# Optimization experiments

Hardware: AMD Instinct MI355X
Metric: run time of the kernel (lower is better)

The kernel has to match this reference:

```python
import jax, jax.numpy as jnp
import numpy as np

L, B, S, D, H, E = 3, 2, 2048, 1024, 16, 4
Dh = D // H  # 64
DF = E * D   # 4096


def _ln(x, g, b, eps=1e-5):
    m = jnp.mean(x, axis=-1, keepdims=True)
    v = jnp.mean(jnp.square(x - m), axis=-1, keepdims=True)
    return (x - m) * jax.lax.rsqrt(v + eps) * g + b


def setup_inputs() -> dict:
    key = jax.random.key(0)
    ks = jax.random.split(key, 12)
    s = 0.02
    f32 = jnp.float32
    return {
        "x":    jax.random.normal(ks[0], (B, S, D), f32),
        "Wq":   jax.random.normal(ks[1], (L, Dh, Dh), f32) * s,
        "Wk":   jax.random.normal(ks[2], (L, Dh, Dh), f32) * s,
        "Wv":   jax.random.normal(ks[3], (L, Dh, Dh), f32) * s,
        "Wo":   jax.random.normal(ks[4], (L, D, D), f32) * s,
        "bo":   jnp.zeros((L, D), f32),
        "ln1_g": jnp.ones((L, D), f32),
        "ln1_b": jnp.zeros((L, D), f32),
        "W1":   jax.random.normal(ks[5], (L, DF, D), f32) * s,
        "b1":   jnp.zeros((L, DF), f32),
        "W2":   jax.random.normal(ks[6], (L, D, DF), f32) * s,
        "b2":   jnp.zeros((L, D), f32),
        "ln2_g": jnp.ones((L, D), f32),
        "ln2_b": jnp.zeros((L, D), f32),
    }


def reference(x, Wq, Wk, Wv, Wo, bo, ln1_g, ln1_b, W1, b1, W2, b2, ln2_g, ln2_b):
    scale = 1.0 / np.sqrt(Dh).astype(np.float32)
    out = x
    for l in range(L):
        xh = out.reshape(B, S, H, Dh)
        # per-head Linear (shared 64x64 weight across heads), torch Linear: y = x @ W.T
        q = jnp.einsum('bshd,ed->bhse', xh, Wq[l])  # [B,H,S,Dh]
        k = jnp.einsum('bshd,ed->bhse', xh, Wk[l])
        v = jnp.einsum('bshd,ed->bhse', xh, Wv[l])
        att = jax.nn.softmax(jnp.einsum('bhse,bhte->bhst', q, k) * scale, axis=-1)
        ctx = jnp.einsum('bhst,bhtd->bshd', att, v).reshape(B, S, D)
        att_out = ctx @ Wo[l].T + bo[l]
        n1 = _ln(att_out + out, ln1_g[l], ln1_b[l])  # residual adds layer input (v == out)
        ff = jax.nn.relu(n1 @ W1[l].T + b1[l]) @ W2[l].T + b2[l]
        out = _ln(ff + n1, ln2_g[l], ln2_b[l])
    return out
```

## Files before the change

### kernel.cpp

```cpp
#include <hip/hip_runtime.h>
#include <hip/hip_bf16.h>
#include <math.h>


#define DEVINL __device__ __forceinline__
typedef unsigned short ushort_t;
using short8 = __attribute__((ext_vector_type(8))) short;
using f32x4  = __attribute__((ext_vector_type(4))) float;

#if defined(__has_builtin)
#if __has_builtin(__builtin_amdgcn_exp2f)
#define EXPFN(x) __builtin_amdgcn_exp2f(x)
#define QSCALE 0.18033688011112042f
#define HAVE_EXP2 1
#endif
#endif
#ifndef HAVE_EXP2
#define EXPFN(x) __expf(x)
#define QSCALE 0.125f
#endif

DEVINL short f2b(float f) {
  unsigned u = __float_as_uint(f);
  u += 0x7fff + ((u >> 16) & 1);
  return (short)(u >> 16);
}
DEVINL unsigned pk2(float a, float b) {
  unsigned ua = __float_as_uint(a), ub = __float_as_uint(b);
  ua += 0x7fff + ((ua >> 16) & 1);
  ub += 0x7fff + ((ub >> 16) & 1);
  return (ua >> 16) | (ub & 0xffff0000u);
}
DEVINL unsigned pkc(float a, float b) {
  float2 f; f.x = a; f.y = b;
  __hip_bfloat162 h = __float22bfloat162_rn(f);
  return *reinterpret_cast<unsigned*>(&h);
}
DEVINL float bl(unsigned u) { return __uint_as_float(u << 16); }
DEVINL float bh(unsigned u) { return __uint_as_float(u & 0xffff0000u); }
DEVINL f32x4 mfma16(short8 a, short8 b, f32x4 c) {
  return __builtin_amdgcn_mfma_f32_16x16x32_bf16(a, b, c, 0, 0, 0);
}

typedef __attribute__((address_space(3))) void lds_void;
typedef __attribute__((address_space(1))) void gbl_void;
DEVINL void gl16(const void* g, void* l) {
  __builtin_amdgcn_global_load_lds((const gbl_void*)(unsigned long long)g,
                                   (lds_void*)(unsigned long long)l, 16, 0, 0);
}
template <int N> DEVINL void waitvm() {
  asm volatile("s_waitcnt vmcnt(%0)" ::"n"(N) : "memory");
}
DEVINL void barrier_raw() { __builtin_amdgcn_s_barrier(); }
DEVINL void sched0() { __builtin_amdgcn_sched_barrier(0); }

__global__ __launch_bounds__(256)
void conv_bf16(const float* __restrict__ src, ushort_t* __restrict__ dst,
               int n8) {
  int i = blockIdx.x * 256 + threadIdx.x;
  const int stride = gridDim.x * 256;
  for (; i < n8; i += stride) {
    float4 a = ((const float4*)src)[2 * i];
    float4 b = ((const float4*)src)[2 * i + 1];
    uint4 o;
    o.x = pk2(a.x, a.y); o.y = pk2(a.z, a.w);
    o.z = pk2(b.x, b.y); o.w = pk2(b.z, b.w);
    ((uint4*)dst)[i] = o;
  }
}

DEVINL float block_sum(float v, float* red) {
#pragma unroll
  for (int off = 32; off > 0; off >>= 1) v += __shfl_xor(v, off, 64);
  if ((threadIdx.x & 63) == 0) red[threadIdx.x >> 6] = v;
  __syncthreads();
  float r = red[0] + red[1] + red[2] + red[3];
  __syncthreads();
  return r;
}

__global__ __launch_bounds__(256)
void ln_dual2(const ushort_t* __restrict__ pa, const ushort_t* __restrict__ pb,
              const float* __restrict__ bias, const float* __restrict__ R,
              const float* __restrict__ g, const float* __restrict__ b,
              float* __restrict__ outf, ushort_t* __restrict__ outb) {
  __shared__ float red[4];
  const size_t base = (size_t)blockIdx.x * 1024 + threadIdx.x * 4;
  uint2 ua = *(const uint2*)(pa + base);
  uint2 ub = *(const uint2*)(pb + base);
  float4 vr = *(const float4*)(R + base);
  float4 vbi = *(const float4*)(bias + threadIdx.x * 4);
  float4 v;
  v.x = bl(ua.x) + bl(ub.x) + vr.x + vbi.x;
  v.y = bh(ua.x) + bh(ub.x) + vr.y + vbi.y;
  v.z = bl(ua.y) + bl(ub.y) + vr.z + vbi.z;
  v.w = bh(ua.y) + bh(ub.y) + vr.w + vbi.w;
  float s = block_sum(v.x + v.y + v.z + v.w, red);
  float mean = s * (1.0f / 1024.0f);
  float dx = v.x - mean, dy = v.y - mean, dz = v.z - mean, dw = v.w - mean;
  float sq = block_sum(dx * dx + dy * dy + dz * dz + dw * dw, red);
  float rstd = rsqrtf(sq * (1.0f / 1024.0f) + 1e-5f);
  const float4 gv = *(const float4*)(g + threadIdx.x * 4);
  const float4 bv = *(const float4*)(b + threadIdx.x * 4);
  float4 o;
  o.x = dx * rstd * gv.x + bv.x;
  o.y = dy * rstd * gv.y + bv.y;
  o.z = dz * rstd * gv.z + bv.z;
  o.w = dw * rstd * gv.w + bv.w;
  *(float4*)(outf + base) = o;
  uint2 p;
  p.x = pk2(o.x, o.y); p.y = pk2(o.z, o.w);
  *(uint2*)(outb + base) = p;
}

template <int BM, int BN, int WR, int WC, bool OBF, int EPI, bool SWZ>
__global__ __launch_bounds__(WR * WC * 64)
void gemm_db(const ushort_t* __restrict__ A, const ushort_t* __restrict__ W,
             const float* __restrict__ bias, void* __restrict__ Cp, int M,
             int N, int Klen, int lda, int ldw) {
  constexpr int THREADS = WR * WC * 64;
  constexpr int FM = BM / WR / 16;
  constexpr int FN = BN / WC / 16;
  constexpr int CA = BM * 8 / THREADS;
  constexpr int CB = BN * 8 / THREADS;
  constexpr int L = CA + CB;
  __shared__ __align__(16) ushort_t As[2][BM * 64];
  __shared__ __align__(16) ushort_t Bs[2][BN * 64];
  const int tid = threadIdx.x;
  const int lane = tid & 63, lo = lane & 15, hi = lane >> 4, w = tid >> 6;
  int bx = blockIdx.x, by = blockIdx.y;
  if (SWZ) {
    int id = by * gridDim.x + bx;
    const int cpx = (gridDim.x * gridDim.y) >> 3;
    id = (id & 7) * cpx + (id >> 3);
    bx = id % gridDim.x;
    by = id / gridDim.x;
  }
  const int m0 = by * BM, n0 = bx * BN;
  const int wm = (w / WC) * (BM / WR), wn = (w % WC) * (BN / WC);
  const int kbase = blockIdx.z * Klen;

  auto stage = [&](int t, int buf) {
    const int k0 = kbase + t * 64;
#pragma unroll
    for (int i = 0; i < CA; ++i) {
      const int c = i * THREADS + tid;
      const int r = c >> 3, sg = (c & 7) ^ (r & 7);
      gl16(A + (size_t)(m0 + r) * lda + k0 + sg * 8, &As[buf][c * 8]);
    }
#pragma unroll
    for (int i = 0; i < CB; ++i) {
      const int c = i * THREADS + tid;
      const int r = c >> 3, sg = (c & 7) ^ (r & 7);
      gl16(W + (size_t)(n0 + r) * ldw + k0 + sg * 8, &Bs[buf][c * 8]);
    }
  };

  f32x4 acc[FM][FN] = {};
  auto compute = [&](int cur) {
#pragma unroll
    for (int ks = 0; ks < 2; ++ks) {
      short8 af[FM], bf_[FN];
#pragma unroll
      for (int fm = 0; fm < FM; ++fm) {
        const int row = wm + fm * 16 + lo;
        af[fm] = *(const short8*)
            &As[cur][row * 64 + (((ks * 4 + hi) ^ (row & 7)) << 3)];
      }
#pragma unroll
      for (int fn = 0; fn < FN; ++fn) {
        const int row = wn + fn * 16 + lo;
        bf_[fn] = *(const short8*)
            &Bs[cur][row * 64 + (((ks * 4 + hi) ^ (row & 7)) << 3)];
      }
#pragma unroll
      for (int fm = 0; fm < FM; ++fm)
#pragma unroll
        for (int fn = 0; fn < FN; ++fn)
          acc[fm][fn] = mfma16(af[fm], bf_[fn], acc[fm][fn]);
    }
  };

  const int nt = Klen / 64;
  stage(0, 0);
  for (int t = 0; t < nt - 1; ++t) {
    const int cur = t & 1;
    stage(t + 1, cur ^ 1);
    waitvm<L>();
    barrier_raw(); sched0();
    compute(cur);
    barrier_raw(); sched0();
  }
  waitvm<0>();
  barrier_raw(); sched0();
  compute((nt - 1) & 1);

  float bv[FN];
#pragma unroll
  for (int fn = 0; fn < FN; ++fn)
    bv[fn] = (EPI & 1) ? bias[n0 + wn + fn * 16 + lo] : 0.f;
#pragma unroll
  for (int fm = 0; fm < FM; ++fm)
#pragma unroll
    for (int fn = 0; fn < FN; ++fn) {
      const int col = n0 + wn + fn * 16 + lo;
#pragma unroll
      for (int r = 0; r < 4; ++r) {
        const int row = m0 + wm + fm * 16 + hi * 4 + r;
        float v = acc[fm][fn][r] + bv[fn];
        if (EPI & 4) v = fmaxf(v, 0.f);
        if (OBF) {
          ushort_t* Cb = (ushort_t*)Cp + (size_t)blockIdx.z * M * N;
          Cb[(size_t)row * N + col] = (ushort_t)f2b(v);
        } else {
          float* Cf = (float*)Cp + (size_t)blockIdx.z * M * N;
          Cf[(size_t)row * N + col] = v;
        }
      }
    }
}

__global__ __launch_bounds__(256)
void qkv_kernel(const ushort_t* __restrict__ A, const ushort_t* __restrict__ Wq,
                const ushort_t* __restrict__ Wk, const ushort_t* __restrict__ Wv,
                ushort_t* __restrict__ q, ushort_t* __restrict__ k,
                ushort_t* __restrict__ v) {
  __shared__ __align__(16) ushort_t As[128 * 64];
  __shared__ __align__(16) ushort_t Ws[3][64 * 64];
  const int tid = threadIdx.x;
  const int lane = tid & 63, lo = lane & 15, hi = lane >> 4, w = tid >> 6;
  const int m0 = blockIdx.x * 128;
  const int wm = (w >> 1) * 64, wn = (w & 1) * 32;

#pragma unroll
  for (int i = 0; i < 4; ++i) {
    const int c = i * 256 + tid;
    const int r = c >> 3, sg = (c & 7) ^ (r & 7);
    gl16(A + (size_t)(m0 + r) * 64 + sg * 8, As + c * 8);
  }
#pragma unroll
  for (int o = 0; o < 3; ++o) {
    const ushort_t* wb = (o == 0) ? Wq : (o == 1) ? Wk : Wv;
#pragma unroll
    for (int i = 0; i < 2; ++i) {
      const int c = i * 256 + tid;
      const int r = c >> 3, sg = (c & 7) ^ (r & 7);
      gl16(wb + (size_t)r * 64 + sg * 8, Ws[o] + c * 8);
    }
  }
  __syncthreads();

#pragma unroll
  for (int o = 0; o < 3; ++o) {
    ushort_t* ob = (o == 0) ? q : (o == 1) ? k : v;
    const float sc = (o == 0) ? QSCALE : 1.0f;
    f32x4 acc[4][2] = {};
#pragma unroll
    for (int ks = 0; ks < 2; ++ks) {
      short8 af[4], bf[2];
#pragma unroll
      for (int fm = 0; fm < 4; ++fm) {
        const int row = wm + fm * 16 + lo;
        af[fm] = *(const short8*)
            &As[row * 64 + (((ks * 4 + hi) ^ (row & 7)) << 3)];
      }
#pragma unroll
      for (int fn = 0; fn < 2; ++fn) {
        const int row = wn + fn * 16 + lo;
        bf[fn] = *(const short8*)
            &Ws[o][row * 64 + (((ks * 4 + hi) ^ (row & 7)) << 3)];
      }
#pragma unroll
      for (int fm = 0; fm < 4; ++fm)
#pragma unroll
        for (int fn = 0; fn < 2; ++fn)
          acc[fm][fn] = mfma16(af[fm], bf[fn], acc[fm][fn]);
    }
#pragma unroll
    for (int fm = 0; fm < 4; ++fm)
#pragma unroll
      for (int fn = 0; fn < 2; ++fn) {
        const int col = wn + fn * 16 + lo;
#pragma unroll
        for (int r = 0; r < 4; ++r) {
          const int row = m0 + wm + fm * 16 + hi * 4 + r;
          size_t idx;
          if (o == 2) {
            idx = (size_t)row * 64 + col;
          } else {
            idx = (size_t)((row >> 15) * 16 + (row & 15)) * 131072 +
                  (size_t)((row >> 4) & 2047) * 64 + col;
          }
          ob[idx] = (ushort_t)f2b(acc[fm][fn][r] * sc);
        }
      }
  }
}

__global__ __launch_bounds__(256)
void vtrans(const ushort_t* __restrict__ V, ushort_t* __restrict__ VT) {
  __shared__ ushort_t T[64][65];
  const int tid = threadIdx.x;
  const int s0 = blockIdx.x * 64, hd0 = blockIdx.y * 64, b = blockIdx.z;
  const ushort_t* src = V + (size_t)b * 2097152;
  ushort_t* dst = VT + (size_t)b * 2097152;
#pragma unroll
  for (int i = 0; i < 2; ++i) {
    int c = tid + i * 256;
    int s = c >> 3, kg = c & 7;
    short8 hv = *(const short8*)(src + (size_t)(s0 + s) * 1024 + hd0 + kg * 8);
#pragma unroll
    for (int j = 0; j < 8; ++j) T[s][kg * 8 + j] = (ushort_t)hv[j];
  }
  __syncthreads();
#pragma unroll
  for (int i = 0; i < 2; ++i) {
    int c = tid + i * 256;
    int hd = c >> 3, sg = c & 7;
    short8 o;
#pragma unroll
    for (int j = 0; j < 8; ++j) o[j] = (short)T[sg * 8 + j][hd];
    *(short8*)(dst + (size_t)(hd0 + hd) * 2048 + s0 + sg * 8) = o;
  }
}

__global__ __launch_bounds__(256)
void attn3(const ushort_t* __restrict__ Qh, const ushort_t* __restrict__ Kh,
           const ushort_t* __restrict__ VT, ushort_t* __restrict__ O) {
  __shared__ __align__(16) ushort_t Kbuf[3][64 * 64];
  __shared__ __align__(16) ushort_t Vbuf[3][64 * 64];
  __shared__ __align__(16) ushort_t Pbuf[4][16 * 40];
  const int tid = threadIdx.x, w = tid >> 6, lane = tid & 63;
  const int lo = lane & 15, hi = lane >> 4;
  const int bh = blockIdx.y, b = bh >> 4, h = bh & 15;
  const size_t hq = (size_t)bh * 131072;
  const size_t vth = (size_t)b * 2097152 + (size_t)h * 131072;
  const size_t oh = (size_t)b * 2097152 + (size_t)h * 64;
  const int qrow = blockIdx.x * 64 + w * 16;
  ushort_t* Pw = Pbuf[w];

  const ushort_t* qp = Qh + hq + (size_t)(qrow + lo) * 64 + hi * 8;
  const short8 qf0 = *(const short8*)qp;
  const short8 qf1 = *(const short8*)(qp + 32);

  const int c0 = tid, c1 = 256 + tid;
  const int r0 = c0 >> 3, s0 = ((c0 & 7) ^ (r0 & 7)) << 3;
  const int r1 = c1 >> 3, s1 = ((c1 & 7) ^ (r1 & 7)) << 3;
  const ushort_t* kg0 = Kh + hq + (size_t)r0 * 64 + s0;
  const ushort_t* kg1 = Kh + hq + (size_t)r1 * 64 + s1;
  const ushort_t* vg0 = VT + vth + (size_t)r0 * 2048 + s0;
  const ushort_t* vg1 = VT + vth + (size_t)r1 * 2048 + s1;

  auto stage = [&](int kt, ushort_t* Kd, ushort_t* Vd) {
    gl16(kg0 + (size_t)kt * 4096, Kd + c0 * 8);
    gl16(kg1 + (size_t)kt * 4096, Kd + c1 * 8);
    gl16(vg0 + kt * 64, Vd + c0 * 8);
    gl16(vg1 + kt * 64, Vd + c1 * 8);
  };

  f32x4 acc[4] = {};
  f32x4 lacc = {};
  const int sw = lo & 7;
  const int ko0 = (hi ^ sw) << 3, ko1 = ((4 + hi) ^ sw) << 3;

  auto body = [&](const ushort_t* Kc, const ushort_t* Vc) {
    f32x4 sc[4];
    __builtin_amdgcn_s_setprio(1);
#pragma unroll
    for (int fm = 0; fm < 4; ++fm) {
      const int rb = (fm * 16 + lo) * 64;
      f32x4 t = {};
      t = mfma16(*(const short8*)&Kc[rb + ko0], qf0, t);
      t = mfma16(*(const short8*)&Kc[rb + ko1], qf1, t);
      sc[fm] = t;
    }
    __builtin_amdgcn_s_setprio(0);
    short8 vf[4][2];
#pragma unroll
    for (int fn = 0; fn < 4; ++fn) {
      const int rb = (fn * 16 + lo) * 64;
      vf[fn][0] = *(const short8*)&Vc[rb + ko0];
      vf[fn][1] = *(const short8*)&Vc[rb + ko1];
    }
#pragma unroll
    for (int fm = 0; fm < 4; ++fm) {
      f32x4 p;
      p[0] = EXPFN(sc[fm][0]); p[1] = EXPFN(sc[fm][1]);
      p[2] = EXPFN(sc[fm][2]); p[3] = EXPFN(sc[fm][3]);
      lacc += p;
      uint2 pw;
      pw.x = pkc(p[0], p[1]); pw.y = pkc(p[2], p[3]);
      *(uint2*)&Pw[lo * 40 + fm * 16 + hi * 4] = pw;
    }
    short8 pb0 = *(const short8*)&Pw[lo * 40 + hi * 8];
    short8 pb1 = *(const short8*)&Pw[lo * 40 + 32 + hi * 8];
    __builtin_amdgcn_s_setprio(1);
#pragma unroll
    for (int fn = 0; fn < 4; ++fn) {
      acc[fn] = mfma16(vf[fn][0], pb0, acc[fn]);
      acc[fn] = mfma16(vf[fn][1], pb1, acc[fn]);
    }
    __builtin_amdgcn_s_setprio(0);
  };

  ushort_t *kA = Kbuf[0], *kB = Kbuf[1], *kC = Kbuf[2];
  ushort_t *vA = Vbuf[0], *vB = Vbuf[1], *vC = Vbuf[2];
  stage(0, kA, vA);
  stage(1, kB, vB);
  for (int kt = 0; kt < 31; ++kt) {
    waitvm<4>();
    barrier_raw(); sched0();
    if (kt < 30) stage(kt + 2, kC, vC);
    body(kA, vA);
    ushort_t* t;
    t = kA; kA = kB; kB = kC; kC = t;
    t = vA; vA = vB; vB = vC; vC = t;
  }
  waitvm<0>();
  barrier_raw(); sched0();
  body(kA, vA);

  float lsum = (lacc[0] + lacc[1]) + (lacc[2] + lacc[3]);
  lsum += __shfl_xor(lsum, 16);
  lsum += __shfl_xor(lsum, 32);
  const float inv = 1.0f / lsum;
  ushort_t* op = O + oh + (size_t)(qrow + lo) * 1024 + hi * 4;
#pragma unroll
  for (int fn = 0; fn < 4; ++fn) {
    uint2 o;
    o.x = pk2(acc[fn][0] * inv, acc[fn][1] * inv);
    o.y = pk2(acc[fn][2] * inv, acc[fn][3] * inv);
    *(uint2*)(op + fn * 16) = o;
  }
}

extern "C" void kernel_launch(void* const* d_in, const int* in_sizes, int n_in,
                              void* d_out, int out_size, void* d_ws,
                              size_t ws_size, hipStream_t stream) {
  const float* x    = (const float*)d_in[0];
  const float* Wq   = (const float*)d_in[1];
  const float* Wk   = (const float*)d_in[2];
  const float* Wv   = (const float*)d_in[3];
  const float* Wo   = (const float*)d_in[4];
  const float* bo   = (const float*)d_in[5];
  const float* ln1g = (const float*)d_in[6];
  const float* ln1b = (const float*)d_in[7];
  const float* W1   = (const float*)d_in[8];
  const float* b1   = (const float*)d_in[9];
  const float* W2   = (const float*)d_in[10];
  const float* b2   = (const float*)d_in[11];
  const float* ln2g = (const float*)d_in[12];
  const float* ln2b = (const float*)d_in[13];
  float* out = (float*)d_out;
  char* wsb = (char*)d_ws;

  ushort_t* t0  = (ushort_t*)wsb;
  ushort_t* t0b = t0 + 4194304;
  ushort_t* q   = (ushort_t*)(wsb + (16ull << 20));
  ushort_t* k   = (ushort_t*)(wsb + (24ull << 20));
  ushort_t* v   = (ushort_t*)(wsb + (32ull << 20));
  ushort_t* vt  = (ushort_t*)(wsb + (40ull << 20));
  ushort_t* ff  = q;
  ushort_t* ctx = (ushort_t*)(wsb + (48ull << 20));
  ushort_t* n1b = ctx;
  ushort_t* xbf = (ushort_t*)(wsb + (56ull << 20));
  ushort_t* wqb = (ushort_t*)(wsb + (64ull << 20));
  ushort_t* wkb = wqb + 3 * 4096;
  ushort_t* wvb = wkb + 3 * 4096;
  ushort_t* wob = (ushort_t*)(wsb + (65ull << 20));
  ushort_t* w1b = (ushort_t*)(wsb + (67ull << 20));
  ushort_t* w2b = (ushort_t*)(wsb + (75ull << 20));

  auto conv = [&](const float* s, ushort_t* d, long n) {
    int n8 = (int)(n / 8);
    int g = (n8 + 255) / 256;
    if (g > 2048) g = 2048;
    conv_bf16<<<g, 256, 0, stream>>>(s, d, n8);
  };
  conv(x, xbf, 4194304);
  conv(Wq, wqb, 3 * 4096);
  conv(Wk, wkb, 3 * 4096);
  conv(Wv, wvb, 3 * 4096);

  const ushort_t* curb = xbf;
  const float* curf = x;
  for (int l = 0; l < 3; ++l) {
    conv(Wo + (size_t)l * 1048576, wob, 1048576);
    conv(W1 + (size_t)l * 4194304, w1b, 4194304);
    conv(W2 + (size_t)l * 4194304, w2b, 4194304);

    qkv_kernel<<<512, 256, 0, stream>>>(curb, wqb + l * 4096, wkb + l * 4096,
                                        wvb + l * 4096, q, k, v);
    vtrans<<<dim3(32, 16, 2), 256, 0, stream>>>(v, vt);
    attn3<<<dim3(32, 32), 256, 0, stream>>>(q, k, vt, ctx);
    gemm_db<128, 64, 2, 2, true, 0, true>
        <<<dim3(16, 32, 2), 256, 0, stream>>>(ctx, wob, nullptr, t0, 4096,
                                              1024, 512, 1024, 1024);
    ln_dual2<<<4096, 256, 0, stream>>>(t0, t0b, bo + l * 1024, curf,
                                       ln1g + l * 1024, ln1b + l * 1024, out,
                                       n1b);
    gemm_db<128, 128, 2, 2, true, 5, true>
        <<<dim3(32, 32, 1), 256, 0, stream>>>(n1b, w1b, b1 + l * 4096, ff,
                                              4096, 4096, 1024, 1024, 1024);
    gemm_db<128, 64, 2, 2, true, 0, true>
        <<<dim3(16, 32, 2), 256, 0, stream>>>(ff, w2b, nullptr, t0, 4096,
                                              1024, 2048, 4096, 4096);
    ln_dual2<<<4096, 256, 0, stream>>>(t0, t0b, b2 + l * 1024, out,
                                       ln2g + l * 1024, ln2b + l * 1024, out,
                                       xbf);
    curb = xbf;
    curf = out;
  }
}
```

Baseline: 635.5 us.

## Use bf16 residuals, batch weight conversion, remap attention grid, double-buffer KV

The layernorm kernels now read the residual from the bf16 copy instead of fp32 and write the fp32 output only on the last layer, cutting global traffic. All layer weights are converted to bf16 in one upfront batch instead of per layer. The attention kernel remaps block indices so consecutive blocks spread across heads, and it drops from triple to double buffering of K/V with an extra barrier per iteration. Using bf16 residuals lowers accuracy, and the extra barrier may reduce load/compute overlap.

```diff
diff --git a/kernel.cpp b/kernel.cpp
--- a/kernel.cpp
+++ b/kernel.cpp
@@ -79,22 +79,23 @@
   return r;
 }
 
+template <bool WF>
 __global__ __launch_bounds__(256)
-void ln_dual2(const ushort_t* __restrict__ pa, const ushort_t* __restrict__ pb,
-              const float* __restrict__ bias, const float* __restrict__ R,
-              const float* __restrict__ g, const float* __restrict__ b,
-              float* __restrict__ outf, ushort_t* __restrict__ outb) {
+void ln_fuse(const ushort_t* __restrict__ pa, const ushort_t* __restrict__ pb,
+             const float* __restrict__ bias, const ushort_t* __restrict__ Rb,
+             const float* __restrict__ g, const float* __restrict__ b,
+             ushort_t* __restrict__ outb, float* __restrict__ outf) {
   __shared__ float red[4];
   const size_t base = (size_t)blockIdx.x * 1024 + threadIdx.x * 4;
   uint2 ua = *(const uint2*)(pa + base);
   uint2 ub = *(const uint2*)(pb + base);
-  float4 vr = *(const float4*)(R + base);
+  uint2 ur = *(const uint2*)(Rb + base);
   float4 vbi = *(const float4*)(bias + threadIdx.x * 4);
   float4 v;
-  v.x = bl(ua.x) + bl(ub.x) + vr.x + vbi.x;
-  v.y = bh(ua.x) + bh(ub.x) + vr.y + vbi.y;
-  v.z = bl(ua.y) + bl(ub.y) + vr.z + vbi.z;
-  v.w = bh(ua.y) + bh(ub.y) + vr.w + vbi.w;
+  v.x = bl(ua.x) + bl(ub.x) + bl(ur.x) + vbi.x;
+  v.y = bh(ua.x) + bh(ub.x) + bh(ur.x) + vbi.y;
+  v.z = bl(ua.y) + bl(ub.y) + bl(ur.y) + vbi.z;
+  v.w = bh(ua.y) + bh(ub.y) + bh(ur.y) + vbi.w;
   float s = block_sum(v.x + v.y + v.z + v.w, red);
   float mean = s * (1.0f / 1024.0f);
   float dx = v.x - mean, dy = v.y - mean, dz = v.z - mean, dw = v.w - mean;
@@ -107,10 +108,10 @@
   o.y = dy * rstd * gv.y + bv.y;
   o.z = dz * rstd * gv.z + bv.z;
   o.w = dw * rstd * gv.w + bv.w;
-  *(float4*)(outf + base) = o;
   uint2 p;
   p.x = pk2(o.x, o.y); p.y = pk2(o.z, o.w);
   *(uint2*)(outb + base) = p;
+  if (WF) *(float4*)(outf + base) = o;
 }
 
 template <int BM, int BN, int WR, int WC, bool OBF, int EPI, bool SWZ>
@@ -327,16 +328,19 @@
 __global__ __launch_bounds__(256)
 void attn3(const ushort_t* __restrict__ Qh, const ushort_t* __restrict__ Kh,
            const ushort_t* __restrict__ VT, ushort_t* __restrict__ O) {
-  __shared__ __align__(16) ushort_t Kbuf[3][64 * 64];
-  __shared__ __align__(16) ushort_t Vbuf[3][64 * 64];
+  __shared__ __align__(16) ushort_t Kbuf[2][64 * 64];
+  __shared__ __align__(16) ushort_t Vbuf[2][64 * 64];
   __shared__ __align__(16) ushort_t Pbuf[4][16 * 40];
   const int tid = threadIdx.x, w = tid >> 6, lane = tid & 63;
   const int lo = lane & 15, hi = lane >> 4;
-  const int bh = blockIdx.y, b = bh >> 4, h = bh & 15;
+  const int hid = blockIdx.y * 32 + blockIdx.x;
+  const int logical = (hid & 7) * 128 + (hid >> 3);
+  const int bh = logical >> 5, qt = logical & 31;
+  const int b = bh >> 4, h = bh & 15;
   const size_t hq = (size_t)bh * 131072;
   const size_t vth = (size_t)b * 2097152 + (size_t)h * 131072;
   const size_t oh = (size_t)b * 2097152 + (size_t)h * 64;
-  const int qrow = blockIdx.x * 64 + w * 16;
+  const int qrow = qt * 64 + w * 16;
   ushort_t* Pw = Pbuf[w];
 
   const ushort_t* qp = Qh + hq + (size_t)(qrow + lo) * 64 + hi * 8;
@@ -351,11 +355,11 @@
   const ushort_t* vg0 = VT + vth + (size_t)r0 * 2048 + s0;
   const ushort_t* vg1 = VT + vth + (size_t)r1 * 2048 + s1;
 
-  auto stage = [&](int kt, ushort_t* Kd, ushort_t* Vd) {
-    gl16(kg0 + (size_t)kt * 4096, Kd + c0 * 8);
-    gl16(kg1 + (size_t)kt * 4096, Kd + c1 * 8);
-    gl16(vg0 + kt * 64, Vd + c0 * 8);
-    gl16(vg1 + kt * 64, Vd + c1 * 8);
+  auto stage = [&](int kt, int buf) {
+    gl16(kg0 + (size_t)kt * 4096, &Kbuf[buf][c0 * 8]);
+    gl16(kg1 + (size_t)kt * 4096, &Kbuf[buf][c1 * 8]);
+    gl16(vg0 + kt * 64, &Vbuf[buf][c0 * 8]);
+    gl16(vg1 + kt * 64, &Vbuf[buf][c1 * 8]);
   };
 
   f32x4 acc[4] = {};
@@ -403,22 +407,17 @@
     __builtin_amdgcn_s_setprio(0);
   };
 
-  ushort_t *kA = Kbuf[0], *kB = Kbuf[1], *kC = Kbuf[2];
-  ushort_t *vA = Vbuf[0], *vB = Vbuf[1], *vC = Vbuf[2];
-  stage(0, kA, vA);
-  stage(1, kB, vB);
+  stage(0, 0);
   for (int kt = 0; kt < 31; ++kt) {
+    stage(kt + 1, (kt + 1) & 1);
     waitvm<4>();
     barrier_raw(); sched0();
-    if (kt < 30) stage(kt + 2, kC, vC);
-    body(kA, vA);
-    ushort_t* t;
-    t = kA; kA = kB; kB = kC; kC = t;
-    t = vA; vA = vB; vB = vC; vC = t;
+    body(Kbuf[kt & 1], Vbuf[kt & 1]);
+    barrier_raw(); sched0();
   }
   waitvm<0>();
   barrier_raw(); sched0();
-  body(kA, vA);
+  body(Kbuf[1], Vbuf[1]);
 
   float lsum = (lacc[0] + lacc[1]) + (lacc[2] + lacc[3]);
   lsum += __shfl_xor(lsum, 16);
@@ -468,8 +467,8 @@
   ushort_t* wkb = wqb + 3 * 4096;
   ushort_t* wvb = wkb + 3 * 4096;
   ushort_t* wob = (ushort_t*)(wsb + (65ull << 20));
-  ushort_t* w1b = (ushort_t*)(wsb + (67ull << 20));
-  ushort_t* w2b = (ushort_t*)(wsb + (75ull << 20));
+  ushort_t* w1b = (ushort_t*)(wsb + (72ull << 20));
+  ushort_t* w2b = (ushort_t*)(wsb + (96ull << 20));
 
   auto conv = [&](const float* s, ushort_t* d, long n) {
     int n8 = (int)(n / 8);
@@ -481,34 +480,39 @@
   conv(Wq, wqb, 3 * 4096);
   conv(Wk, wkb, 3 * 4096);
   conv(Wv, wvb, 3 * 4096);
+  conv(Wo, wob, 3ll * 1048576);
+  conv(W1, w1b, 3ll * 4194304);
+  conv(W2, w2b, 3ll * 4194304);
 
   const ushort_t* curb = xbf;
-  const float* curf = x;
   for (int l = 0; l < 3; ++l) {
-    conv(Wo + (size_t)l * 1048576, wob, 1048576);
-    conv(W1 + (size_t)l * 4194304, w1b, 4194304);
-    conv(W2 + (size_t)l * 4194304, w2b, 4194304);
-
     qkv_kernel<<<512, 256, 0, stream>>>(curb, wqb + l * 4096, wkb + l * 4096,
                                         wvb + l * 4096, q, k, v);
     vtrans<<<dim3(32, 16, 2), 256, 0, stream>>>(v, vt);
     attn3<<<dim3(32, 32), 256, 0, stream>>>(q, k, vt, ctx);
     gemm_db<128, 64, 2, 2, true, 0, true>
-        <<<dim3(16, 32, 2), 256, 0, stream>>>(ctx, wob, nullptr, t0, 4096,
-                                              1024, 512, 1024, 1024);
-    ln_dual2<<<4096, 256, 0, stream>>>(t0, t0b, bo + l * 1024, curf,
-                                       ln1g + l * 1024, ln1b + l * 1024, out,
-                                       n1b);
+        <<<dim3(16, 32, 2), 256, 0, stream>>>(ctx, wob + (size_t)l * 1048576,
+                                              nullptr, t0, 4096, 1024, 512,
+                                              1024, 1024);
+    ln_fuse<false><<<4096, 256, 0, stream>>>(t0, t0b, bo + l * 1024, curb,
+                                             ln1g + l * 1024, ln1b + l * 1024,
+                                             n1b, nullptr);
     gemm_db<128, 128, 2, 2, true, 5, true>
-        <<<dim3(32, 32, 1), 256, 0, stream>>>(n1b, w1b, b1 + l * 4096, ff,
-                                              4096, 4096, 1024, 1024, 1024);
+        <<<dim3(32, 32, 1), 256, 0, stream>>>(n1b, w1b + (size_t)l * 4194304,
+                                              b1 + l * 4096, ff, 4096, 4096,
+                                              1024, 1024, 1024);
     gemm_db<128, 64, 2, 2, true, 0, true>
-        <<<dim3(16, 32, 2), 256, 0, stream>>>(ff, w2b, nullptr, t0, 4096,
-                                              1024, 2048, 4096, 4096);
-    ln_dual2<<<4096, 256, 0, stream>>>(t0, t0b, b2 + l * 1024, out,
-                                       ln2g + l * 1024, ln2b + l * 1024, out,
-                                       xbf);
+        <<<dim3(16, 32, 2), 256, 0, stream>>>(ff, w2b + (size_t)l * 4194304,
+                                              nullptr, t0, 4096, 1024, 2048,
+                                              4096, 4096);
+    if (l == 2)
+      ln_fuse<true><<<4096, 256, 0, stream>>>(t0, t0b, b2 + l * 1024, n1b,
+                                              ln2g + l * 1024, ln2b + l * 1024,
+                                              xbf, out);
+    else
+      ln_fuse<false><<<4096, 256, 0, stream>>>(t0, t0b, b2 + l * 1024, n1b,
+                                               ln2g + l * 1024, ln2b + l * 1024,
+                                               xbf, nullptr);
     curb = xbf;
-    curf = out;
-  }
-}
+  }
+}
```

After: 608.1 us. -4.3%, faster.
